# Optimization experiments

Hardware: AMD Instinct MI355X
Metric: run time of the kernel (lower is better)

## Reference

```python
import jax, jax.numpy as jnp
import numpy as np
import math

B, S, DIM = 2, 2048, 2048
H, NOPE, ROPE, VDIM = 16, 128, 64, 128
Q_RANK, KV_RANK = 1024, 512
EPS = 1e-6
ROPE_THETA = 10000.0


def setup_inputs() -> dict:
    key = jax.random.key(0)
    ks = jax.random.split(key, 9)
    s = 0.02  # init scale to keep activations/logits well-conditioned
    return {
        "x": jax.random.normal(ks[0], (B, S, DIM), jnp.float32),
        "wq_down": jax.random.normal(ks[1], (Q_RANK, DIM), jnp.float32) * s,
        "q_norm_w": jnp.ones((Q_RANK,), jnp.float32),
        "wq_up": jax.random.normal(ks[2], (H * NOPE, Q_RANK), jnp.float32) * s,
        "wq_rope": jax.random.normal(ks[3], (H * ROPE, Q_RANK), jnp.float32) * s,
        "wkv_down": jax.random.normal(ks[4], (KV_RANK, DIM), jnp.float32) * s,
        "kv_norm_w": jnp.ones((KV_RANK,), jnp.float32),
        "wkv_up": jax.random.normal(ks[5], (H * (NOPE + VDIM), KV_RANK), jnp.float32) * s,
        "wk_rope": jax.random.normal(ks[6], (ROPE, DIM), jnp.float32) * s,
        "wo": jax.random.normal(ks[7], (DIM, H * VDIM), jnp.float32) * s,
    }


def _rmsnorm(x, w, eps=EPS):
    return x * jax.lax.rsqrt(jnp.mean(x * x, axis=-1, keepdims=True) + eps) * w


def _rope_cos_sin(seq_len, head_dim, dtype=jnp.float32):
    inv_freq = 1.0 / (ROPE_THETA ** (jnp.arange(0, head_dim, 2, dtype=jnp.float32) / head_dim))
    t = jnp.arange(seq_len, dtype=jnp.float32)
    freqs = jnp.outer(t, inv_freq)  # [S, head_dim/2]
    return jnp.cos(freqs).astype(dtype), jnp.sin(freqs).astype(dtype)


def _apply_rope(x, cos, sin):
    # x: [B, S, h, d]; cos/sin: [S, d/2]; interleaved (complex) rotation
    x1, x2 = x[..., 0::2], x[..., 1::2]
    c = cos[None, :, None, :]
    s = sin[None, :, None, :]
    o1 = x1 * c - x2 * s
    o2 = x1 * s + x2 * c
    return jnp.stack([o1, o2], axis=-1).reshape(x.shape)


def reference(x, wq_down, q_norm_w, wq_up, wq_rope, wkv_down, kv_norm_w, wkv_up, wk_rope, wo):
    bs, seq_len, _ = x.shape
    # low-rank Q path
    q_c = _rmsnorm(x @ wq_down.T, q_norm_w)                       # [B,S,Qr]
    q_nope = (q_c @ wq_up.T).reshape(bs, seq_len, H, NOPE)
    q_pe = (q_c @ wq_rope.T).reshape(bs, seq_len, H, ROPE)
    # low-rank KV path
    kv_c = _rmsnorm(x @ wkv_down.T, kv_norm_w)                    # [B,S,KVr]
    kv_up = (x_kv := kv_c @ wkv_up.T).reshape(bs, seq_len, H, NOPE + VDIM)
    k_nope, v = kv_up[..., :NOPE], kv_up[..., NOPE:]
    k_rope_shared = (x @ wk_rope.T).reshape(bs, seq_len, 1, ROPE)
    # decoupled RoPE
    cos, sin = _rope_cos_sin(seq_len, ROPE, x.dtype)
    q_pe = _apply_rope(q_pe, cos, sin)
    k_rope_shared = _apply_rope(k_rope_shared, cos, sin)
    k_rope = jnp.broadcast_to(k_rope_shared, (bs, seq_len, H, ROPE))
    q = jnp.concatenate([q_nope, q_pe], axis=-1)                  # [B,S,H,NOPE+ROPE]
    k = jnp.concatenate([k_nope, k_rope], axis=-1)
    scale = 1.0 / math.sqrt(NOPE + ROPE)
    scores = jnp.einsum("bqhd,bkhd->bhqk", q, k) * scale          # [B,H,S,S]
    causal = jnp.tril(jnp.ones((seq_len, seq_len), bool))
    scores = jnp.where(causal[None, None], scores, -jnp.inf)
    probs = jax.nn.softmax(scores.astype(jnp.float32), axis=-1).astype(q.dtype)
    out = jnp.einsum("bhqk,bkhv->bqhv", probs, v).reshape(bs, seq_len, H * VDIM)
    return out @ wo.T
```

## Files before the change

### kernel.cpp

```cpp
#include <hip/hip_runtime.h>
#include <hip/hip_bf16.h>
#include <math.h>

#define B_    2
#define S_    2048
#define DIM_  2048
#define H_    16
#define NOPE_ 128
#define ROPE_ 64
#define VDIM_ 128
#define QR_   1024
#define KVR_  512
#define TOK_  (B_ * S_)

typedef __attribute__((ext_vector_type(8))) short short8;
typedef __attribute__((ext_vector_type(4))) float f32x4;

__device__ __forceinline__ unsigned short f2bf(float f) {
  union { float f; unsigned u; } v; v.f = f;
  unsigned r = v.u + 0x7fffu + ((v.u >> 16) & 1u);
  return (unsigned short)(r >> 16);
}
__device__ __forceinline__ unsigned pk2(float lo, float hi) {
  return (unsigned)f2bf(lo) | ((unsigned)f2bf(hi) << 16);
}

__device__ __forceinline__ void gl_lds16(const unsigned short* g, unsigned short* lds_base) {
  __builtin_amdgcn_global_load_lds(
      (const __attribute__((address_space(1))) void*)g,
      (__attribute__((address_space(3))) void*)lds_base,
      16, 0, 0);
}

__device__ __forceinline__ void store_out(float* p, float v) { *p = v; }
__device__ __forceinline__ void store_out(unsigned short* p, float v) { *p = f2bf(v); }

#define C_X    (TOK_ * DIM_ / 8)
#define C_WQD  (QR_ * DIM_ / 8)
#define C_WKVD (KVR_ * DIM_ / 8)
#define C_WKR  (ROPE_ * DIM_ / 8)
#define C_WQU  (H_ * NOPE_ * QR_ / 8)
#define C_WQR  (H_ * ROPE_ * QR_ / 8)
#define C_WKVU (H_ * (NOPE_ + VDIM_) * KVR_ / 8)
#define C_WO   (DIM_ * H_ * VDIM_ / 8)
#define C_TOT  (C_X + C_WQD + C_WKVD + C_WKR + C_WQU + C_WQR + C_WKVU + C_WO)

__global__ __launch_bounds__(256) void cvt_all(
    const float* __restrict__ x, const float* __restrict__ wqd, const float* __restrict__ wkvd,
    const float* __restrict__ wkr, const float* __restrict__ wqu, const float* __restrict__ wqr,
    const float* __restrict__ wkvu, const float* __restrict__ wo,
    unsigned short* __restrict__ xo, unsigned short* __restrict__ wqdo,
    unsigned short* __restrict__ wkvdo, unsigned short* __restrict__ wkro,
    unsigned short* __restrict__ wquo, unsigned short* __restrict__ wqro,
    unsigned short* __restrict__ wkvuo, unsigned short* __restrict__ woo) {
  int i = blockIdx.x * 256 + threadIdx.x;
  if (i >= C_TOT) return;
  const float* in; unsigned short* out;
  if (i < C_X) { in = x; out = xo; }
  else if ((i -= C_X) < C_WQD) { in = wqd; out = wqdo; }
  else if ((i -= C_WQD) < C_WKVD) { in = wkvd; out = wkvdo; }
  else if ((i -= C_WKVD) < C_WKR) { in = wkr; out = wkro; }
  else if ((i -= C_WKR) < C_WQU) { in = wqu; out = wquo; }
  else if ((i -= C_WQU) < C_WQR) { in = wqr; out = wqro; }
  else if ((i -= C_WQR) < C_WKVU) { in = wkvu; out = wkvuo; }
  else { i -= C_WKVU; in = wo; out = woo; }
  float4 f0 = *(const float4*)(in + (size_t)i * 8);
  float4 f1 = *(const float4*)(in + (size_t)i * 8 + 4);
  uint4 u;
  u.x = pk2(f0.x, f0.y); u.y = pk2(f0.z, f0.w);
  u.z = pk2(f1.x, f1.y); u.w = pk2(f1.z, f1.w);
  *(uint4*)&out[(size_t)i * 8] = u;
}

template <typename OutT, int NT>
__global__ __launch_bounds__(256) void gemm_bf16(const unsigned short* __restrict__ A,
                                                 const unsigned short* __restrict__ Bm,
                                                 OutT* __restrict__ C,
                                                 int M, int N, int K) {
  constexpr int BN = NT * 32;
  __shared__ unsigned short As[128 * 32];
  __shared__ unsigned short Bs[BN * 32];
  const int tid  = threadIdx.x;
  const int wave = tid >> 6;
  const int lane = tid & 63;
  const int quad = lane >> 4;
  const int l15  = lane & 15;
  const int m0 = blockIdx.y * 128;
  const int n0 = blockIdx.x * BN;
  const int wm = (wave & 1) * 64;
  const int wn = (wave >> 1) * (NT * 16);

  f32x4 acc[4][NT];
#pragma unroll
  for (int i = 0; i < 4; ++i)
#pragma unroll
    for (int j = 0; j < NT; ++j) {
      f32x4 z = {0.f, 0.f, 0.f, 0.f};
      acc[i][j] = z;
    }

  for (int k0 = 0; k0 < K; k0 += 32) {
    __syncthreads();
#pragma unroll
    for (int i = 0; i < 2; ++i) {
      const int s = i * 256 + tid;
      const int srow = s >> 2;
      const int sq = (s & 3) ^ ((srow >> 1) & 3);
      gl_lds16(A + (size_t)(m0 + srow) * K + k0 + sq * 8, &As[(i * 256 + wave * 64) * 8]);
    }
#pragma unroll
    for (int i = 0; i < BN / 64; ++i) {
      const int s = i * 256 + tid;
      const int srow = s >> 2;
      const int sq = (s & 3) ^ ((srow >> 1) & 3);
      const int rb = min(n0 + srow, N - 1);
      gl_lds16(Bm + (size_t)rb * K + k0 + sq * 8, &Bs[(i * 256 + wave * 64) * 8]);
    }
    __syncthreads();

    short8 a[4], b[NT];
#pragma unroll
    for (int i = 0; i < 4; ++i) {
      const int r = wm + i * 16 + l15;
      a[i] = *(const short8*)&As[(r * 4 + (quad ^ ((r >> 1) & 3))) * 8];
    }
#pragma unroll
    for (int j = 0; j < NT; ++j) {
      const int r = wn + j * 16 + l15;
      b[j] = *(const short8*)&Bs[(r * 4 + (quad ^ ((r >> 1) & 3))) * 8];
    }
#pragma unroll
    for (int i = 0; i < 4; ++i)
#pragma unroll
      for (int j = 0; j < NT; ++j)
        acc[i][j] = __builtin_amdgcn_mfma_f32_16x16x32_bf16(a[i], b[j], acc[i][j], 0, 0, 0);
  }

#pragma unroll
  for (int i = 0; i < 4; ++i) {
#pragma unroll
    for (int j = 0; j < NT; ++j) {
      const int col = n0 + wn + j * 16 + l15;
      if (col < N) {
#pragma unroll
        for (int r = 0; r < 4; ++r) {
          const int row = m0 + wm + i * 16 + quad * 4 + r;
          store_out(&C[(size_t)row * N + col], acc[i][j][r]);
        }
      }
    }
  }
}

__global__ __launch_bounds__(256) void gemm_down(const unsigned short* __restrict__ A,
                                                 const unsigned short* __restrict__ Bq,
                                                 const unsigned short* __restrict__ Bkv,
                                                 const unsigned short* __restrict__ Bkr,
                                                 float* __restrict__ Cq,
                                                 float* __restrict__ Ckv,
                                                 float* __restrict__ Ckr) {
  constexpr int K = DIM_;
  __shared__ unsigned short As[128 * 32];
  __shared__ unsigned short Bs[128 * 32];
  const int tid  = threadIdx.x;
  const int wave = tid >> 6;
  const int lane = tid & 63;
  const int quad = lane >> 4;
  const int l15  = lane & 15;
  const int m0 = blockIdx.y * 128;
  const int t  = blockIdx.x;

  const unsigned short* Bm; float* C; int n0, NB;
  if (t < 8)       { Bm = Bq;  C = Cq;  n0 = t * 128;        NB = QR_;  }
  else if (t < 12) { Bm = Bkv; C = Ckv; n0 = (t - 8) * 128;  NB = KVR_; }
  else             { Bm = Bkr; C = Ckr; n0 = 0;              NB = ROPE_; }

  const int wm = (wave & 1) * 64;
  const int wn = (wave >> 1) * 64;

  f32x4 acc[4][4];
#pragma unroll
  for (int i = 0; i < 4; ++i)
#pragma unroll
    for (int j = 0; j < 4; ++j) { f32x4 z = {0.f, 0.f, 0.f, 0.f}; acc[i][j] = z; }

  for (int k0 = 0; k0 < K; k0 += 32) {
    __syncthreads();
#pragma unroll
    for (int i = 0; i < 2; ++i) {
      const int s = i * 256 + tid;
      const int srow = s >> 2;
      const int sq = (s & 3) ^ ((srow >> 1) & 3);
      gl_lds16(A + (size_t)(m0 + srow) * K + k0 + sq * 8, &As[(i * 256 + wave * 64) * 8]);
    }
#pragma unroll
    for (int i = 0; i < 2; ++i) {
      const int s = i * 256 + tid;
      const int srow = s >> 2;
      const int sq = (s & 3) ^ ((srow >> 1) & 3);
      const int rb = min(n0 + srow, NB - 1);
      gl_lds16(Bm + (size_t)rb * K + k0 + sq * 8, &Bs[(i * 256 + wave * 64) * 8]);
    }
    __syncthreads();

    short8 a[4], b[4];
#pragma unroll
    for (int i = 0; i < 4; ++i) {
      const int r = wm + i * 16 + l15;
      a[i] = *(const short8*)&As[(r * 4 + (quad ^ ((r >> 1) & 3))) * 8];
    }
#pragma unroll
    for (int j = 0; j < 4; ++j) {
      const int r = wn + j * 16 + l15;
      b[j] = *(const short8*)&Bs[(r * 4 + (quad ^ ((r >> 1) & 3))) * 8];
    }
#pragma unroll
    for (int i = 0; i < 4; ++i)
#pragma unroll
      for (int j = 0; j < 4; ++j)
        acc[i][j] = __builtin_amdgcn_mfma_f32_16x16x32_bf16(a[i], b[j], acc[i][j], 0, 0, 0);
  }

#pragma unroll
  for (int i = 0; i < 4; ++i) {
#pragma unroll
    for (int j = 0; j < 4; ++j) {
      const int col = n0 + wn + j * 16 + l15;
      if (col < NB) {
#pragma unroll
        for (int r = 0; r < 4; ++r) {
          const int row = m0 + wm + i * 16 + quad * 4 + r;
          C[(size_t)row * NB + col] = acc[i][j][r];
        }
      }
    }
  }
}

__global__ __launch_bounds__(256) void gemm_upq(const unsigned short* __restrict__ A,
                                                const unsigned short* __restrict__ Bn,
                                                const unsigned short* __restrict__ Br,
                                                unsigned short* __restrict__ Cn,
                                                float* __restrict__ Cr) {
  constexpr int K = QR_;
  __shared__ unsigned short As[128 * 32];
  __shared__ unsigned short Bs[128 * 32];
  const int tid  = threadIdx.x;
  const int wave = tid >> 6;
  const int lane = tid & 63;
  const int quad = lane >> 4;
  const int l15  = lane & 15;
  const int m0 = blockIdx.y * 128;
  const int t  = blockIdx.x;
  const bool isn = (t < 16);
  const unsigned short* Bm = isn ? Bn : Br;
  const int n0 = isn ? t * 128 : (t - 16) * 128;
  const int NB = isn ? (H_ * NOPE_) : (H_ * ROPE_);

  const int wm = (wave & 1) * 64;
  const int wn = (wave >> 1) * 64;

  f32x4 acc[4][4];
#pragma unroll
  for (int i = 0; i < 4; ++i)
#pragma unroll
    for (int j = 0; j < 4; ++j) { f32x4 z = {0.f, 0.f, 0.f, 0.f}; acc[i][j] = z; }

  for (int k0 = 0; k0 < K; k0 += 32) {
    __syncthreads();
#pragma unroll
    for (int i = 0; i < 2; ++i) {
      const int s = i * 256 + tid;
      const int srow = s >> 2;
      const int sq = (s & 3) ^ ((srow >> 1) & 3);
      gl_lds16(A + (size_t)(m0 + srow) * K + k0 + sq * 8, &As[(i * 256 + wave * 64) * 8]);
    }
#pragma unroll
    for (int i = 0; i < 2; ++i) {
      const int s = i * 256 + tid;
      const int srow = s >> 2;
      const int sq = (s & 3) ^ ((srow >> 1) & 3);
      const int rb = min(n0 + srow, NB - 1);
      gl_lds16(Bm + (size_t)rb * K + k0 + sq * 8, &Bs[(i * 256 + wave * 64) * 8]);
    }
    __syncthreads();

    short8 a[4], b[4];
#pragma unroll
    for (int i = 0; i < 4; ++i) {
      const int r = wm + i * 16 + l15;
      a[i] = *(const short8*)&As[(r * 4 + (quad ^ ((r >> 1) & 3))) * 8];
    }
#pragma unroll
    for (int j = 0; j < 4; ++j) {
      const int r = wn + j * 16 + l15;
      b[j] = *(const short8*)&Bs[(r * 4 + (quad ^ ((r >> 1) & 3))) * 8];
    }
#pragma unroll
    for (int i = 0; i < 4; ++i)
#pragma unroll
      for (int j = 0; j < 4; ++j)
        acc[i][j] = __builtin_amdgcn_mfma_f32_16x16x32_bf16(a[i], b[j], acc[i][j], 0, 0, 0);
  }

#pragma unroll
  for (int i = 0; i < 4; ++i) {
#pragma unroll
    for (int j = 0; j < 4; ++j) {
      const int col = n0 + wn + j * 16 + l15;
#pragma unroll
      for (int r = 0; r < 4; ++r) {
        const int row = m0 + wm + i * 16 + quad * 4 + r;
        if (isn) Cn[(size_t)row * (H_ * NOPE_) + col] = f2bf(acc[i][j][r]);
        else     Cr[(size_t)row * (H_ * ROPE_) + col] = acc[i][j][r];
      }
    }
  }
}

__global__ __launch_bounds__(256) void rmsnorm2(const float* __restrict__ xq,
                                                const float* __restrict__ wq,
                                                unsigned short* __restrict__ oq,
                                                const float* __restrict__ xkv,
                                                const float* __restrict__ wkv,
                                                unsigned short* __restrict__ okv) {
  __shared__ float red[256];
  const bool isq = (blockIdx.y == 0);
  const int n = isq ? QR_ : KVR_;
  const float* x = isq ? xq : xkv;
  const float* w = isq ? wq : wkv;
  unsigned short* o = isq ? oq : okv;
  const int row = blockIdx.x;
  const float* p = x + (size_t)row * n;
  float s = 0.f;
  for (int i = threadIdx.x; i < n; i += 256) { float v = p[i]; s += v * v; }
  red[threadIdx.x] = s;
  __syncthreads();
  for (int off = 128; off > 0; off >>= 1) {
    if (threadIdx.x < off) red[threadIdx.x] += red[threadIdx.x + off];
    __syncthreads();
  }
  const float inv = rsqrtf(red[0] / (float)n + 1e-6f);
  unsigned short* po = o + (size_t)row * n;
  for (int i = threadIdx.x; i < n; i += 256) po[i] = f2bf(p[i] * inv * w[i]);
}

#define PAIRS_Q (TOK_ * H_ * 32)
#define PAIRS_K (TOK_ * 32)

__global__ void rope_all(const float* __restrict__ qin, unsigned short* __restrict__ qout,
                         const float* __restrict__ kin, unsigned short* __restrict__ kout) {
  int idx = blockIdx.x * blockDim.x + threadIdx.x;
  if (idx >= PAIRS_Q + PAIRS_K) return;
  int heads, id;
  const float* xin; unsigned short* xout;
  if (idx < PAIRS_Q) { heads = H_; xin = qin; xout = qout; id = idx; }
  else { heads = 1; xin = kin; xout = kout; id = idx - PAIRS_Q; }
  const int i = id & 31;
  const int h = (id >> 5) % heads;
  const int row = id / (32 * heads);
  const int pos = row & (S_ - 1);
  const float freq = expf(-9.210340371976184f * (float)i / 32.0f);
  const float ang = (float)pos * freq;
  const float c = cosf(ang), sn = sinf(ang);
  const float* p = xin + ((size_t)row * heads + h) * 64 + 2 * i;
  unsigned short* q = xout + ((size_t)row * heads + h) * 64 + 2 * i;
  const float x1 = p[0], x2 = p[1];
  q[0] = f2bf(x1 * c - x2 * sn);
  q[1] = f2bf(x1 * sn + x2 * c);
}

__global__ __launch_bounds__(256) void transpose_v(const unsigned short* __restrict__ kv_up,
                                                   unsigned short* __restrict__ vt_g) {
  __shared__ unsigned short T[128 * 72];
  const int tid = threadIdx.x;
  const int k0 = blockIdx.x * 64;
  const int h = blockIdx.y, b = blockIdx.z;
  const size_t tok0 = (size_t)b * S_;
#pragma unroll
  for (int i = 0; i < 2; ++i) {
    const int u = i * 256 + tid;
    const int kp = u >> 4, c8 = u & 15;
    const unsigned short* p0 =
        kv_up + (tok0 + k0 + 2 * kp) * (size_t)(H_ * 256) + h * 256 + NOPE_ + c8 * 8;
    union { uint4 v; unsigned short s[8]; } r0, r1;
    r0.v = *(const uint4*)p0;
    r1.v = *(const uint4*)(p0 + H_ * 256);
#pragma unroll
    for (int j = 0; j < 8; ++j)
      *(unsigned*)&T[(c8 * 8 + j) * 72 + 2 * kp] = (unsigned)r0.s[j] | ((unsigned)r1.s[j] << 16);
  }
  __syncthreads();
#pragma unroll
  for (int i = 0; i < 4; ++i) {
    const int sl = i * 256 + tid;
    const int f = sl >> 3, c = sl & 7;
    *(uint4*)(vt_g + ((size_t)(b * H_ + h) * 128 + f) * S_ + k0 + c * 8) =
        *(const uint4*)&T[f * 72 + c * 8];
  }
}

#define LV 72

__global__ __launch_bounds__(512) void flash_attn_mfma(const unsigned short* q_nope,
                                                       const unsigned short* __restrict__ q_pe,
                                                       const unsigned short* __restrict__ kv_up,
                                                       const unsigned short* __restrict__ k_rope,
                                                       const unsigned short* __restrict__ vt_g,
                                                       unsigned short* attn_o) {
  __shared__ unsigned short Ksn[2][128 * 16 * 8];
  __shared__ unsigned short Ksr[2][128 * 8 * 8];
  __shared__ unsigned short Vt[128 * 16 * 8];
  __shared__ unsigned short Ps[128 * LV];

  const int tid  = threadIdx.x;
  const int wave = tid >> 6;
  const int lane = tid & 63;
  const int quad = lane >> 4;
  const int l15  = lane & 15;
  const int l   = blockIdx.x + 8 * blockIdx.y + 128 * blockIdx.z;
  const int c_  = l & 7;
  const int m_  = l >> 3;
  const int pair = m_ & 7;
  const int hb   = c_ * 4 + (m_ >> 3);
  const int h  = hb & 15;
  const int b  = hb >> 4;
  const size_t tok0 = (size_t)b * S_;
  const float scale2 = 0.07216878364870323f * 1.4426950408889634f;
  const int qtA = 15 - pair;
  const int qtB = pair;
  const int nA  = qtA + 1;

  auto LOADQ = [&](short8* qf, int qt) {
    const size_t qrow = tok0 + qt * 128 + wave * 16 + l15;
    const unsigned short* pn = q_nope + qrow * (size_t)(H_ * NOPE_) + h * NOPE_;
    const unsigned short* pp = q_pe + qrow * (size_t)(H_ * ROPE_) + h * ROPE_;
#pragma unroll
    for (int s = 0; s < 4; ++s) qf[s] = *(const short8*)(pn + s * 32 + quad * 8);
#pragma unroll
    for (int s = 4; s < 6; ++s) qf[s] = *(const short8*)(pp + (s - 4) * 32 + quad * 8);
  };

  auto STAGE_K = [&](int bi, int kt) {
    const int k0 = kt * 128;
#pragma unroll
    for (int i = 0; i < 4; ++i) {
      const int sl = i * 512 + tid;
      const int key = sl >> 4;
      const int c = (sl & 15) ^ (key & 15);
      gl_lds16(kv_up + (tok0 + k0 + key) * (size_t)(H_ * 256) + h * 256 + c * 8,
               &Ksn[bi][(i * 512 + wave * 64) * 8]);
    }
#pragma unroll
    for (int i = 0; i < 2; ++i) {
      const int sl = i * 512 + tid;
      const int key = sl >> 3;
      const int c = (sl & 7) ^ (key & 7);
      gl_lds16(k_rope + (tok0 + k0 + key) * (size_t)ROPE_ + c * 8,
               &Ksr[bi][(i * 512 + wave * 64) * 8]);
    }
  };
  auto STAGE_V = [&](int kt) {
    const int k0 = kt * 128;
#pragma unroll
    for (int i = 0; i < 4; ++i) {
      const int sl = i * 512 + tid;
      const int f = sl >> 4;
      const int c = (sl & 15) ^ (f & 15);
      gl_lds16(vt_g + ((size_t)(b * H_ + h) * 128 + f) * S_ + k0 + c * 8,
               &Vt[(i * 512 + wave * 64) * 8]);
    }
  };

  short8 qf[6];
  LOADQ(qf, qtA);

  float m_st[4], l_st[4];
  f32x4 o[8];
#pragma unroll
  for (int r = 0; r < 4; ++r) { m_st[r] = -1e30f; l_st[r] = 0.f; }
#pragma unroll
  for (int nt = 0; nt < 8; ++nt) { f32x4 z = {0.f, 0.f, 0.f, 0.f}; o[nt] = z; }

  auto EPI = [&](int qt) {
    float invl[4];
#pragma unroll
    for (int r = 0; r < 4; ++r) invl[r] = 1.f / l_st[r];
#pragma unroll
    for (int nt = 0; nt < 8; ++nt)
#pragma unroll
      for (int r = 0; r < 4; ++r) {
        const size_t row = tok0 + qt * 128 + wave * 16 + quad * 4 + r;
        attn_o[row * (size_t)(H_ * VDIM_) + h * VDIM_ + nt * 16 + l15] =
            f2bf(o[nt][r] * invl[r]);
      }
  };

  STAGE_K(0, 0);

  for (int it = 0; it < 17; ++it) {
    const int cur = it & 1;
    const int nxt = cur ^ 1;
    const bool ph1 = (it >= nA);
    const int qt = ph1 ? qtB : qtA;
    const int kt = ph1 ? (it - nA) : it;
    const bool last = (it + 1 >= 17);

    __builtin_amdgcn_s_barrier();
    asm volatile("" ::: "memory");

    STAGE_V(kt);
    if (!last) {
      const int it2 = it + 1;
      const int kt2 = (it2 >= nA) ? (it2 - nA) : it2;
      STAGE_K(nxt, kt2);
      asm volatile("s_waitcnt vmcnt(10)" ::: "memory");
    } else {
      asm volatile("s_waitcnt vmcnt(4)" ::: "memory");
    }
    __builtin_amdgcn_s_barrier();
    asm volatile("" ::: "memory");
    __builtin_amdgcn_sched_barrier(0);

    f32x4 sacc[8];
#pragma unroll
    for (int nt = 0; nt < 8; ++nt) { f32x4 z = {0.f, 0.f, 0.f, 0.f}; sacc[nt] = z; }
    __builtin_amdgcn_s_setprio(1);
#pragma unroll
    for (int s = 0; s < 4; ++s) {
#pragma unroll
      for (int nt = 0; nt < 8; ++nt) {
        const int key = nt * 16 + l15;
        short8 kb = *(const short8*)&Ksn[cur][(key * 16 + ((s * 4 + quad) ^ (key & 15))) * 8];
        sacc[nt] = __builtin_amdgcn_mfma_f32_16x16x32_bf16(qf[s], kb, sacc[nt], 0, 0, 0);
      }
    }
#pragma unroll
    for (int s = 4; s < 6; ++s) {
#pragma unroll
      for (int nt = 0; nt < 8; ++nt) {
        const int key = nt * 16 + l15;
        short8 kb = *(const short8*)&Ksr[cur][(key * 8 + (((s - 4) * 4 + quad) ^ (key & 7))) * 8];
        sacc[nt] = __builtin_amdgcn_mfma_f32_16x16x32_bf16(qf[s], kb, sacc[nt], 0, 0, 0);
      }
    }
    __builtin_amdgcn_s_setprio(0);

    float sc[8][4];
#pragma unroll
    for (int nt = 0; nt < 8; ++nt)
#pragma unroll
      for (int r = 0; r < 4; ++r) sc[nt][r] = sacc[nt][r] * scale2;
    if (kt == qt) {
      const int rw = wave * 16 + quad * 4;
#pragma unroll
      for (int nt = 0; nt < 8; ++nt)
#pragma unroll
        for (int r = 0; r < 4; ++r)
          if ((nt * 16 + l15) > (rw + r)) sc[nt][r] = -1e30f;
    }

    float mt[4];
#pragma unroll
    for (int r = 0; r < 4; ++r) {
      float a0 = fmaxf(fmaxf(sc[0][r], sc[1][r]), fmaxf(sc[2][r], sc[3][r]));
      float a1 = fmaxf(fmaxf(sc[4][r], sc[5][r]), fmaxf(sc[6][r], sc[7][r]));
      mt[r] = fmaxf(a0, a1);
    }
#pragma unroll
    for (int mask = 1; mask <= 8; mask <<= 1)
#pragma unroll
      for (int r = 0; r < 4; ++r) mt[r] = fmaxf(mt[r], __shfl_xor(mt[r], mask, 64));

    float al[4], rs[4];
#pragma unroll
    for (int r = 0; r < 4; ++r) {
      const float mn = fmaxf(m_st[r], mt[r]);
      al[r] = exp2f(m_st[r] - mn);
      m_st[r] = mn;
      rs[r] = 0.f;
    }
#pragma unroll
    for (int nt = 0; nt < 8; ++nt)
#pragma unroll
      for (int r = 0; r < 4; ++r) {
        const float p = exp2f(sc[nt][r] - m_st[r]);
        sc[nt][r] = p;
        rs[r] += p;
      }
#pragma unroll
    for (int mask = 1; mask <= 8; mask <<= 1)
#pragma unroll
      for (int r = 0; r < 4; ++r) rs[r] += __shfl_xor(rs[r], mask, 64);
#pragma unroll
    for (int r = 0; r < 4; ++r) l_st[r] = l_st[r] * al[r] + rs[r];

#pragma unroll
    for (int nt = 0; nt < 4; ++nt)
#pragma unroll
      for (int r = 0; r < 4; ++r)
        Ps[(wave * 16 + quad * 4 + r) * LV + nt * 16 + l15] = f2bf(sc[nt][r]);
    __builtin_amdgcn_wave_barrier();

#pragma unroll
    for (int nt = 0; nt < 8; ++nt)
#pragma unroll
      for (int r = 0; r < 4; ++r) o[nt][r] *= al[r];

    if (!last) {
      asm volatile("s_waitcnt vmcnt(6)" ::: "memory");
    } else {
      asm volatile("s_waitcnt vmcnt(0)" ::: "memory");
    }
    __builtin_amdgcn_s_barrier();
    asm volatile("" ::: "memory");
    __builtin_amdgcn_sched_barrier(0);

    __builtin_amdgcn_s_setprio(1);
#pragma unroll
    for (int kb = 0; kb < 2; ++kb) {
      short8 pa = *(const short8*)&Ps[(wave * 16 + l15) * LV + kb * 32 + quad * 8];
#pragma unroll
      for (int nt = 0; nt < 8; ++nt) {
        const int f = nt * 16 + l15;
        short8 vb = *(const short8*)&Vt[(f * 16 + ((kb * 4 + quad) ^ (f & 15))) * 8];
        o[nt] = __builtin_amdgcn_mfma_f32_16x16x32_bf16(pa, vb, o[nt], 0, 0, 0);
      }
    }
    __builtin_amdgcn_s_setprio(0);

#pragma unroll
    for (int nt = 4; nt < 8; ++nt)
#pragma unroll
      for (int r = 0; r < 4; ++r)
        Ps[(wave * 16 + quad * 4 + r) * LV + (nt - 4) * 16 + l15] = f2bf(sc[nt][r]);
    __builtin_amdgcn_wave_barrier();

    __builtin_amdgcn_s_setprio(1);
#pragma unroll
    for (int kb = 2; kb < 4; ++kb) {
      short8 pa = *(const short8*)&Ps[(wave * 16 + l15) * LV + (kb - 2) * 32 + quad * 8];
#pragma unroll
      for (int nt = 0; nt < 8; ++nt) {
        const int f = nt * 16 + l15;
        short8 vb = *(const short8*)&Vt[(f * 16 + ((kb * 4 + quad) ^ (f & 15))) * 8];
        o[nt] = __builtin_amdgcn_mfma_f32_16x16x32_bf16(pa, vb, o[nt], 0, 0, 0);
      }
    }
    __builtin_amdgcn_s_setprio(0);

    if (it == nA - 1) {
      EPI(qtA);
      LOADQ(qf, qtB);
#pragma unroll
      for (int r = 0; r < 4; ++r) { m_st[r] = -1e30f; l_st[r] = 0.f; }
#pragma unroll
      for (int nt = 0; nt < 8; ++nt) { f32x4 z = {0.f, 0.f, 0.f, 0.f}; o[nt] = z; }
    }
  }

  EPI(qtB);
}

extern "C" void kernel_launch(void* const* d_in, const int* in_sizes, int n_in,
                              void* d_out, int out_size, void* d_ws, size_t ws_size,
                              hipStream_t stream) {
  (void)in_sizes; (void)n_in;
  const float* x         = (const float*)d_in[0];
  const float* wq_down   = (const float*)d_in[1];
  const float* q_norm_w  = (const float*)d_in[2];
  const float* wq_up     = (const float*)d_in[3];
  const float* wq_rope   = (const float*)d_in[4];
  const float* wkv_down  = (const float*)d_in[5];
  const float* kv_norm_w = (const float*)d_in[6];
  const float* wkv_up    = (const float*)d_in[7];
  const float* wk_rope   = (const float*)d_in[8];
  const float* wo        = (const float*)d_in[9];
  float* out = (float*)d_out;

  const size_t SZ_XBF   = (size_t)TOK_ * DIM_ * 2;
  const size_t SZ_WQD   = (size_t)QR_ * DIM_ * 2;
  const size_t SZ_WKVD  = (size_t)KVR_ * DIM_ * 2;
  const size_t SZ_WKR   = (size_t)ROPE_ * DIM_ * 2;
  const size_t SZ_WQU   = (size_t)H_ * NOPE_ * QR_ * 2;
  const size_t SZ_WQR   = (size_t)H_ * ROPE_ * QR_ * 2;
  const size_t SZ_WKVU  = (size_t)H_ * (NOPE_ + VDIM_) * KVR_ * 2;
  const size_t SZ_WO    = (size_t)DIM_ * H_ * VDIM_ * 2;
  const size_t SZ_QC    = (size_t)TOK_ * QR_ * 4;
  const size_t SZ_KVC   = (size_t)TOK_ * KVR_ * 4;
  const size_t SZ_QCN   = (size_t)TOK_ * QR_ * 2;
  const size_t SZ_KVCN  = (size_t)TOK_ * KVR_ * 2;
  const size_t SZ_QNOPE = (size_t)TOK_ * H_ * NOPE_ * 2;
  const size_t SZ_QPEB  = (size_t)TOK_ * H_ * ROPE_ * 2;
  const size_t SZ_KRF   = (size_t)TOK_ * ROPE_ * 4;
  const size_t SZ_KRB   = (size_t)TOK_ * ROPE_ * 2;
  const size_t SZ_KVUP  = (size_t)TOK_ * H_ * (NOPE_ + VDIM_) * 2;
  const size_t NEED = SZ_XBF + SZ_WQD + SZ_WKVD + SZ_WKR + SZ_WQU + SZ_WQR + SZ_WKVU +
                      SZ_WO + SZ_QC + SZ_KVC + SZ_QCN + SZ_KVCN + SZ_QNOPE + SZ_QPEB +
                      SZ_KRF + SZ_KRB + SZ_KVUP;
  if (ws_size < NEED) {
    hipMemsetAsync(d_out, 0, (size_t)out_size * sizeof(float), stream);
    return;
  }
  char* p = (char*)d_ws;
  unsigned short* x_bf    = (unsigned short*)p; p += SZ_XBF;
  unsigned short* wqd_bf  = (unsigned short*)p; p += SZ_WQD;
  unsigned short* wkvd_bf = (unsigned short*)p; p += SZ_WKVD;
  unsigned short* wkr_bf  = (unsigned short*)p; p += SZ_WKR;
  unsigned short* wqu_bf  = (unsigned short*)p; p += SZ_WQU;
  unsigned short* wqr_bf  = (unsigned short*)p; p += SZ_WQR;
  unsigned short* wkvu_bf = (unsigned short*)p; p += SZ_WKVU;
  unsigned short* wo_bf   = (unsigned short*)p; p += SZ_WO;
  float*          q_c     = (float*)p;          p += SZ_QC;
  float*          kv_c    = (float*)p;          p += SZ_KVC;
  unsigned short* q_cn    = (unsigned short*)p; p += SZ_QCN;
  unsigned short* kv_cn   = (unsigned short*)p; p += SZ_KVCN;
  unsigned short* q_nope  = (unsigned short*)p; p += SZ_QNOPE;
  unsigned short* q_pe_bf = (unsigned short*)p; p += SZ_QPEB;
  float*          k_ropef = (float*)p;          p += SZ_KRF;
  unsigned short* k_ropeb = (unsigned short*)p; p += SZ_KRB;
  unsigned short* kv_upbf = (unsigned short*)p; p += SZ_KVUP;
  float*          q_pe_f  = q_c;
  unsigned short* vt_g    = (unsigned short*)q_c;
  unsigned short* attn_o  = q_nope;

  const dim3 blk(256);

  cvt_all<<<(C_TOT + 255) / 256, blk, 0, stream>>>(
      x, wq_down, wkv_down, wk_rope, wq_up, wq_rope, wkv_up, wo,
      x_bf, wqd_bf, wkvd_bf, wkr_bf, wqu_bf, wqr_bf, wkvu_bf, wo_bf);

  gemm_down<<<dim3(13, TOK_ / 128), blk, 0, stream>>>(x_bf, wqd_bf, wkvd_bf, wkr_bf,
                                                      q_c, kv_c, k_ropef);

  rmsnorm2<<<dim3(TOK_, 2), blk, 0, stream>>>(q_c, q_norm_w, q_cn, kv_c, kv_norm_w, kv_cn);

  gemm_upq<<<dim3(24, TOK_ / 128), blk, 0, stream>>>(q_cn, wqu_bf, wqr_bf, q_nope, q_pe_f);

  gemm_bf16<unsigned short, 4><<<dim3(H_ * (NOPE_ + VDIM_) / 128, TOK_ / 128), blk, 0, stream>>>(
      kv_cn, wkvu_bf, kv_upbf, TOK_, H_ * (NOPE_ + VDIM_), KVR_);

  rope_all<<<(PAIRS_Q + PAIRS_K + 255) / 256, blk, 0, stream>>>(q_pe_f, q_pe_bf, k_ropef, k_ropeb);

  transpose_v<<<dim3(S_ / 64, H_, B_), blk, 0, stream>>>(kv_upbf, vt_g);

  flash_attn_mfma<<<dim3(8, H_, B_), dim3(512), 0, stream>>>(q_nope, q_pe_bf, kv_upbf, k_ropeb, vt_g, attn_o);

  gemm_bf16<float, 4><<<dim3(DIM_ / 128, TOK_ / 128), blk, 0, stream>>>(attn_o, wo_bf, out, TOK_, DIM_, H_ * VDIM_);
}
```

Before: 439.6 us.

## Replace GEMMs with double-buffered 128x256 tile core and merged up-projection launch

Introduces a shared GEMM core with 128x256 tiles, 512 threads, BK=64, an 8-way XOR LDS swizzle and double-buffered global_load_lds. The next K-tile is prefetched while MFMAs run on the current one, synchronised with explicit vmcnt waits and raised wave priority around the MFMA block. The down, up and output projections all use this core, and the q-up, q-rope and kv-up GEMMs are merged into one launch. The aim is to hide global-load latency, halve barrier count per K, and improve operand reuse. In exchange, LDS use and register pressure go up, and the 64-wide rope output now gets a mostly padded 256-wide tile.

Measured after the change: 426.8 us. 2.9% less time.

```diff
diff --git a/kernel.cpp b/kernel.cpp
--- a/kernel.cpp
+++ b/kernel.cpp
@@ -31,9 +31,6 @@
       (__attribute__((address_space(3))) void*)lds_base,
       16, 0, 0);
 }
-
-__device__ __forceinline__ void store_out(float* p, float v) { *p = v; }
-__device__ __forceinline__ void store_out(unsigned short* p, float v) { *p = f2bf(v); }
 
 #define C_X    (TOK_ * DIM_ / 8)
 #define C_WQD  (QR_ * DIM_ / 8)
@@ -72,157 +69,111 @@
   *(uint4*)&out[(size_t)i * 8] = u;
 }
 
-template <typename OutT, int NT>
-__global__ __launch_bounds__(256) void gemm_bf16(const unsigned short* __restrict__ A,
-                                                 const unsigned short* __restrict__ Bm,
-                                                 OutT* __restrict__ C,
-                                                 int M, int N, int K) {
-  constexpr int BN = NT * 32;
-  __shared__ unsigned short As[128 * 32];
-  __shared__ unsigned short Bs[BN * 32];
+__device__ __forceinline__ void gemm_core_128x256(
+    const unsigned short* __restrict__ A, const unsigned short* __restrict__ Bm,
+    int K, int NB, int m0, int n0,
+    unsigned short (*As)[128 * 64], unsigned short (*Bs)[256 * 64],
+    f32x4 acc[4][4]) {
   const int tid  = threadIdx.x;
   const int wave = tid >> 6;
   const int lane = tid & 63;
   const int quad = lane >> 4;
   const int l15  = lane & 15;
+  const int wm = (wave & 1) * 64;
+  const int wn = (wave >> 1) * 64;
+
+  auto STAGE = [&](int bi, int k0) {
+#pragma unroll
+    for (int i = 0; i < 2; ++i) {
+      const int s = i * 512 + tid;
+      const int row = s >> 3;
+      const int c = (s & 7) ^ (row & 7);
+      gl_lds16(A + (size_t)(m0 + row) * K + k0 + c * 8, &As[bi][(i * 512 + wave * 64) * 8]);
+    }
+#pragma unroll
+    for (int i = 0; i < 4; ++i) {
+      const int s = i * 512 + tid;
+      const int row = s >> 3;
+      const int c = (s & 7) ^ (row & 7);
+      const int rb = min(n0 + row, NB - 1);
+      gl_lds16(Bm + (size_t)rb * K + k0 + c * 8, &Bs[bi][(i * 512 + wave * 64) * 8]);
+    }
+  };
+
+#pragma unroll
+  for (int i = 0; i < 4; ++i)
+#pragma unroll
+    for (int j = 0; j < 4; ++j) { f32x4 z = {0.f, 0.f, 0.f, 0.f}; acc[i][j] = z; }
+
+  const int nk = K >> 6;
+  STAGE(0, 0);
+  for (int kk = 0; kk < nk; ++kk) {
+    const int cur = kk & 1;
+    __builtin_amdgcn_s_barrier();
+    asm volatile("" ::: "memory");
+    if (kk + 1 < nk) {
+      STAGE(cur ^ 1, (kk + 1) * 64);
+      asm volatile("s_waitcnt vmcnt(6)" ::: "memory");
+    } else {
+      asm volatile("s_waitcnt vmcnt(0)" ::: "memory");
+    }
+    __builtin_amdgcn_s_barrier();
+    asm volatile("" ::: "memory");
+    __builtin_amdgcn_sched_barrier(0);
+
+    short8 a[2][4], b[2][4];
+#pragma unroll
+    for (int s = 0; s < 2; ++s) {
+#pragma unroll
+      for (int i = 0; i < 4; ++i) {
+        const int r = wm + i * 16 + l15;
+        a[s][i] = *(const short8*)&As[cur][(r * 8 + ((s * 4 + quad) ^ (r & 7))) * 8];
+      }
+#pragma unroll
+      for (int j = 0; j < 4; ++j) {
+        const int r = wn + j * 16 + l15;
+        b[s][j] = *(const short8*)&Bs[cur][(r * 8 + ((s * 4 + quad) ^ (r & 7))) * 8];
+      }
+    }
+    __builtin_amdgcn_s_setprio(1);
+#pragma unroll
+    for (int s = 0; s < 2; ++s)
+#pragma unroll
+      for (int i = 0; i < 4; ++i)
+#pragma unroll
+        for (int j = 0; j < 4; ++j)
+          acc[i][j] = __builtin_amdgcn_mfma_f32_16x16x32_bf16(a[s][i], b[s][j], acc[i][j], 0, 0, 0);
+    __builtin_amdgcn_s_setprio(0);
+  }
+}
+
+__global__ __launch_bounds__(512) void gemm_down_p(const unsigned short* __restrict__ A,
+                                                   const unsigned short* __restrict__ Bq,
+                                                   const unsigned short* __restrict__ Bkv,
+                                                   const unsigned short* __restrict__ Bkr,
+                                                   float* __restrict__ Cq,
+                                                   float* __restrict__ Ckv,
+                                                   float* __restrict__ Ckr) {
+  __shared__ unsigned short As[2][128 * 64];
+  __shared__ unsigned short Bs[2][256 * 64];
+  const int t  = blockIdx.x;
   const int m0 = blockIdx.y * 128;
-  const int n0 = blockIdx.x * BN;
-  const int wm = (wave & 1) * 64;
-  const int wn = (wave >> 1) * (NT * 16);
-
-  f32x4 acc[4][NT];
-#pragma unroll
-  for (int i = 0; i < 4; ++i)
-#pragma unroll
-    for (int j = 0; j < NT; ++j) {
-      f32x4 z = {0.f, 0.f, 0.f, 0.f};
-      acc[i][j] = z;
-    }
-
-  for (int k0 = 0; k0 < K; k0 += 32) {
-    __syncthreads();
-#pragma unroll
-    for (int i = 0; i < 2; ++i) {
-      const int s = i * 256 + tid;
-      const int srow = s >> 2;
-      const int sq = (s & 3) ^ ((srow >> 1) & 3);
-      gl_lds16(A + (size_t)(m0 + srow) * K + k0 + sq * 8, &As[(i * 256 + wave * 64) * 8]);
-    }
-#pragma unroll
-    for (int i = 0; i < BN / 64; ++i) {
-      const int s = i * 256 + tid;
-      const int srow = s >> 2;
-      const int sq = (s & 3) ^ ((srow >> 1) & 3);
-      const int rb = min(n0 + srow, N - 1);
-      gl_lds16(Bm + (size_t)rb * K + k0 + sq * 8, &Bs[(i * 256 + wave * 64) * 8]);
-    }
-    __syncthreads();
-
-    short8 a[4], b[NT];
-#pragma unroll
-    for (int i = 0; i < 4; ++i) {
-      const int r = wm + i * 16 + l15;
-      a[i] = *(const short8*)&As[(r * 4 + (quad ^ ((r >> 1) & 3))) * 8];
-    }
-#pragma unroll
-    for (int j = 0; j < NT; ++j) {
-      const int r = wn + j * 16 + l15;
-      b[j] = *(const short8*)&Bs[(r * 4 + (quad ^ ((r >> 1) & 3))) * 8];
-    }
-#pragma unroll
-    for (int i = 0; i < 4; ++i)
-#pragma unroll
-      for (int j = 0; j < NT; ++j)
-        acc[i][j] = __builtin_amdgcn_mfma_f32_16x16x32_bf16(a[i], b[j], acc[i][j], 0, 0, 0);
-  }
-
-#pragma unroll
-  for (int i = 0; i < 4; ++i) {
-#pragma unroll
-    for (int j = 0; j < NT; ++j) {
-      const int col = n0 + wn + j * 16 + l15;
-      if (col < N) {
-#pragma unroll
-        for (int r = 0; r < 4; ++r) {
-          const int row = m0 + wm + i * 16 + quad * 4 + r;
-          store_out(&C[(size_t)row * N + col], acc[i][j][r]);
-        }
-      }
-    }
-  }
-}
-
-__global__ __launch_bounds__(256) void gemm_down(const unsigned short* __restrict__ A,
-                                                 const unsigned short* __restrict__ Bq,
-                                                 const unsigned short* __restrict__ Bkv,
-                                                 const unsigned short* __restrict__ Bkr,
-                                                 float* __restrict__ Cq,
-                                                 float* __restrict__ Ckv,
-                                                 float* __restrict__ Ckr) {
-  constexpr int K = DIM_;
-  __shared__ unsigned short As[128 * 32];
-  __shared__ unsigned short Bs[128 * 32];
-  const int tid  = threadIdx.x;
-  const int wave = tid >> 6;
-  const int lane = tid & 63;
+  const unsigned short* Bm; float* C; int n0, NB;
+  if (t < 4)      { Bm = Bq;  C = Cq;  n0 = t * 256;        NB = QR_;  }
+  else if (t < 6) { Bm = Bkv; C = Ckv; n0 = (t - 4) * 256;  NB = KVR_; }
+  else            { Bm = Bkr; C = Ckr; n0 = 0;              NB = ROPE_; }
+
+  f32x4 acc[4][4];
+  gemm_core_128x256(A, Bm, DIM_, NB, m0, n0, As, Bs, acc);
+
+  const int lane = threadIdx.x & 63;
+  const int wave = threadIdx.x >> 6;
   const int quad = lane >> 4;
   const int l15  = lane & 15;
-  const int m0 = blockIdx.y * 128;
-  const int t  = blockIdx.x;
-
-  const unsigned short* Bm; float* C; int n0, NB;
-  if (t < 8)       { Bm = Bq;  C = Cq;  n0 = t * 128;        NB = QR_;  }
-  else if (t < 12) { Bm = Bkv; C = Ckv; n0 = (t - 8) * 128;  NB = KVR_; }
-  else             { Bm = Bkr; C = Ckr; n0 = 0;              NB = ROPE_; }
-
   const int wm = (wave & 1) * 64;
   const int wn = (wave >> 1) * 64;
-
-  f32x4 acc[4][4];
 #pragma unroll
   for (int i = 0; i < 4; ++i)
-#pragma unroll
-    for (int j = 0; j < 4; ++j) { f32x4 z = {0.f, 0.f, 0.f, 0.f}; acc[i][j] = z; }
-
-  for (int k0 = 0; k0 < K; k0 += 32) {
-    __syncthreads();
-#pragma unroll
-    for (int i = 0; i < 2; ++i) {
-      const int s = i * 256 + tid;
-      const int srow = s >> 2;
-      const int sq = (s & 3) ^ ((srow >> 1) & 3);
-      gl_lds16(A + (size_t)(m0 + srow) * K + k0 + sq * 8, &As[(i * 256 + wave * 64) * 8]);
-    }
-#pragma unroll
-    for (int i = 0; i < 2; ++i) {
-      const int s = i * 256 + tid;
-      const int srow = s >> 2;
-      const int sq = (s & 3) ^ ((srow >> 1) & 3);
-      const int rb = min(n0 + srow, NB - 1);
-      gl_lds16(Bm + (size_t)rb * K + k0 + sq * 8, &Bs[(i * 256 + wave * 64) * 8]);
-    }
-    __syncthreads();
-
-    short8 a[4], b[4];
-#pragma unroll
-    for (int i = 0; i < 4; ++i) {
-      const int r = wm + i * 16 + l15;
-      a[i] = *(const short8*)&As[(r * 4 + (quad ^ ((r >> 1) & 3))) * 8];
-    }
-#pragma unroll
-    for (int j = 0; j < 4; ++j) {
-      const int r = wn + j * 16 + l15;
-      b[j] = *(const short8*)&Bs[(r * 4 + (quad ^ ((r >> 1) & 3))) * 8];
-    }
-#pragma unroll
-    for (int i = 0; i < 4; ++i)
-#pragma unroll
-      for (int j = 0; j < 4; ++j)
-        acc[i][j] = __builtin_amdgcn_mfma_f32_16x16x32_bf16(a[i], b[j], acc[i][j], 0, 0, 0);
-  }
-
-#pragma unroll
-  for (int i = 0; i < 4; ++i) {
 #pragma unroll
     for (int j = 0; j < 4; ++j) {
       const int col = n0 + wn + j * 16 + l15;
@@ -234,88 +185,77 @@
         }
       }
     }
-  }
-}
-
-__global__ __launch_bounds__(256) void gemm_upq(const unsigned short* __restrict__ A,
-                                                const unsigned short* __restrict__ Bn,
-                                                const unsigned short* __restrict__ Br,
-                                                unsigned short* __restrict__ Cn,
-                                                float* __restrict__ Cr) {
-  constexpr int K = QR_;
-  __shared__ unsigned short As[128 * 32];
-  __shared__ unsigned short Bs[128 * 32];
-  const int tid  = threadIdx.x;
-  const int wave = tid >> 6;
-  const int lane = tid & 63;
+}
+
+__global__ __launch_bounds__(512) void gemm_up_p(const unsigned short* __restrict__ Aq,
+                                                 const unsigned short* __restrict__ Akv,
+                                                 const unsigned short* __restrict__ Bn,
+                                                 const unsigned short* __restrict__ Br,
+                                                 const unsigned short* __restrict__ Bkv,
+                                                 unsigned short* __restrict__ Cn,
+                                                 float* __restrict__ Cr,
+                                                 unsigned short* __restrict__ Ckv) {
+  __shared__ unsigned short As[2][128 * 64];
+  __shared__ unsigned short Bs[2][256 * 64];
+  const int t  = blockIdx.x;
+  const int m0 = blockIdx.y * 128;
+  const unsigned short* A; const unsigned short* Bm; int K, n0, NB, mode;
+  if (t < 8)       { A = Aq;  Bm = Bn;  K = QR_;  n0 = t * 256;         NB = H_ * NOPE_;           mode = 0; }
+  else if (t < 12) { A = Aq;  Bm = Br;  K = QR_;  n0 = (t - 8) * 256;   NB = H_ * ROPE_;           mode = 1; }
+  else             { A = Akv; Bm = Bkv; K = KVR_; n0 = (t - 12) * 256;  NB = H_ * (NOPE_ + VDIM_); mode = 2; }
+
+  f32x4 acc[4][4];
+  gemm_core_128x256(A, Bm, K, NB, m0, n0, As, Bs, acc);
+
+  const int lane = threadIdx.x & 63;
+  const int wave = threadIdx.x >> 6;
   const int quad = lane >> 4;
   const int l15  = lane & 15;
-  const int m0 = blockIdx.y * 128;
-  const int t  = blockIdx.x;
-  const bool isn = (t < 16);
-  const unsigned short* Bm = isn ? Bn : Br;
-  const int n0 = isn ? t * 128 : (t - 16) * 128;
-  const int NB = isn ? (H_ * NOPE_) : (H_ * ROPE_);
-
   const int wm = (wave & 1) * 64;
   const int wn = (wave >> 1) * 64;
-
-  f32x4 acc[4][4];
 #pragma unroll
   for (int i = 0; i < 4; ++i)
-#pragma unroll
-    for (int j = 0; j < 4; ++j) { f32x4 z = {0.f, 0.f, 0.f, 0.f}; acc[i][j] = z; }
-
-  for (int k0 = 0; k0 < K; k0 += 32) {
-    __syncthreads();
-#pragma unroll
-    for (int i = 0; i < 2; ++i) {
-      const int s = i * 256 + tid;
-      const int srow = s >> 2;
-      const int sq = (s & 3) ^ ((srow >> 1) & 3);
-      gl_lds16(A + (size_t)(m0 + srow) * K + k0 + sq * 8, &As[(i * 256 + wave * 64) * 8]);
-    }
-#pragma unroll
-    for (int i = 0; i < 2; ++i) {
-      const int s = i * 256 + tid;
-      const int srow = s >> 2;
-      const int sq = (s & 3) ^ ((srow >> 1) & 3);
-      const int rb = min(n0 + srow, NB - 1);
-      gl_lds16(Bm + (size_t)rb * K + k0 + sq * 8, &Bs[(i * 256 + wave * 64) * 8]);
-    }
-    __syncthreads();
-
-    short8 a[4], b[4];
-#pragma unroll
-    for (int i = 0; i < 4; ++i) {
-      const int r = wm + i * 16 + l15;
-      a[i] = *(const short8*)&As[(r * 4 + (quad ^ ((r >> 1) & 3))) * 8];
-    }
-#pragma unroll
-    for (int j = 0; j < 4; ++j) {
-      const int r = wn + j * 16 + l15;
-      b[j] = *(const short8*)&Bs[(r * 4 + (quad ^ ((r >> 1) & 3))) * 8];
-    }
-#pragma unroll
-    for (int i = 0; i < 4; ++i)
-#pragma unroll
-      for (int j = 0; j < 4; ++j)
-        acc[i][j] = __builtin_amdgcn_mfma_f32_16x16x32_bf16(a[i], b[j], acc[i][j], 0, 0, 0);
-  }
-
-#pragma unroll
-  for (int i = 0; i < 4; ++i) {
 #pragma unroll
     for (int j = 0; j < 4; ++j) {
       const int col = n0 + wn + j * 16 + l15;
 #pragma unroll
       for (int r = 0; r < 4; ++r) {
         const int row = m0 + wm + i * 16 + quad * 4 + r;
-        if (isn) Cn[(size_t)row * (H_ * NOPE_) + col] = f2bf(acc[i][j][r]);
-        else     Cr[(size_t)row * (H_ * ROPE_) + col] = acc[i][j][r];
-      }
-    }
-  }
+        if (mode == 0)      Cn[(size_t)row * (H_ * NOPE_) + col] = f2bf(acc[i][j][r]);
+        else if (mode == 1) Cr[(size_t)row * (H_ * ROPE_) + col] = acc[i][j][r];
+        else                Ckv[(size_t)row * (H_ * (NOPE_ + VDIM_)) + col] = f2bf(acc[i][j][r]);
+      }
+    }
+}
+
+__global__ __launch_bounds__(512) void gemm_out_p(const unsigned short* __restrict__ A,
+                                                  const unsigned short* __restrict__ Bm,
+                                                  float* __restrict__ C) {
+  __shared__ unsigned short As[2][128 * 64];
+  __shared__ unsigned short Bs[2][256 * 64];
+  const int n0 = blockIdx.x * 256;
+  const int m0 = blockIdx.y * 128;
+
+  f32x4 acc[4][4];
+  gemm_core_128x256(A, Bm, H_ * VDIM_, DIM_, m0, n0, As, Bs, acc);
+
+  const int lane = threadIdx.x & 63;
+  const int wave = threadIdx.x >> 6;
+  const int quad = lane >> 4;
+  const int l15  = lane & 15;
+  const int wm = (wave & 1) * 64;
+  const int wn = (wave >> 1) * 64;
+#pragma unroll
+  for (int i = 0; i < 4; ++i)
+#pragma unroll
+    for (int j = 0; j < 4; ++j) {
+      const int col = n0 + wn + j * 16 + l15;
+#pragma unroll
+      for (int r = 0; r < 4; ++r) {
+        const int row = m0 + wm + i * 16 + quad * 4 + r;
+        C[(size_t)row * DIM_ + col] = acc[i][j][r];
+      }
+    }
 }
 
 __global__ __launch_bounds__(256) void rmsnorm2(const float* __restrict__ xq,
@@ -730,15 +670,13 @@
       x, wq_down, wkv_down, wk_rope, wq_up, wq_rope, wkv_up, wo,
       x_bf, wqd_bf, wkvd_bf, wkr_bf, wqu_bf, wqr_bf, wkvu_bf, wo_bf);
 
-  gemm_down<<<dim3(13, TOK_ / 128), blk, 0, stream>>>(x_bf, wqd_bf, wkvd_bf, wkr_bf,
-                                                      q_c, kv_c, k_ropef);
+  gemm_down_p<<<dim3(7, TOK_ / 128), dim3(512), 0, stream>>>(x_bf, wqd_bf, wkvd_bf, wkr_bf,
+                                                             q_c, kv_c, k_ropef);
 
   rmsnorm2<<<dim3(TOK_, 2), blk, 0, stream>>>(q_c, q_norm_w, q_cn, kv_c, kv_norm_w, kv_cn);
 
-  gemm_upq<<<dim3(24, TOK_ / 128), blk, 0, stream>>>(q_cn, wqu_bf, wqr_bf, q_nope, q_pe_f);
-
-  gemm_bf16<unsigned short, 4><<<dim3(H_ * (NOPE_ + VDIM_) / 128, TOK_ / 128), blk, 0, stream>>>(
-      kv_cn, wkvu_bf, kv_upbf, TOK_, H_ * (NOPE_ + VDIM_), KVR_);
+  gemm_up_p<<<dim3(28, TOK_ / 128), dim3(512), 0, stream>>>(q_cn, kv_cn, wqu_bf, wqr_bf, wkvu_bf,
+                                                            q_nope, q_pe_f, kv_upbf);
 
   rope_all<<<(PAIRS_Q + PAIRS_K + 255) / 256, blk, 0, stream>>>(q_pe_f, q_pe_bf, k_ropef, k_ropeb);
 
@@ -746,5 +684,5 @@
 
   flash_attn_mfma<<<dim3(8, H_, B_), dim3(512), 0, stream>>>(q_nope, q_pe_bf, kv_upbf, k_ropeb, vt_g, attn_o);
 
-  gemm_bf16<float, 4><<<dim3(DIM_ / 128, TOK_ / 128), blk, 0, stream>>>(attn_o, wo_bf, out, TOK_, DIM_, H_ * VDIM_);
-}
+  gemm_out_p<<<dim3(8, TOK_ / 128), dim3(512), 0, stream>>>(attn_o, wo_bf, out);
+}
```
